# Kernel tuning notes

Measured on AMD Instinct MI355X. Metric: run time of the kernel, lower is better.

Reference implementation:

```python
import jax, jax.numpy as jnp
import numpy as np

C_IN = 256
C_RED = max(4, C_IN // 4)  # 64


def setup_inputs() -> dict:
    key = jax.random.key(0)
    k1, k2, k3, k4, k5 = jax.random.split(key, 5)
    B, C, H, W = 4, C_IN, 64, 64
    x = jax.random.normal(k1, (B, C, H, W), dtype=jnp.float32)
    # 1x1 convs (no bias) are just channel matmuls: weight shape (out_ch, in_ch)
    s_in = 1.0 / np.sqrt(C)
    s_red = 1.0 / np.sqrt(C_RED)
    Wq = jax.random.normal(k2, (C_RED, C), dtype=jnp.float32) * s_in
    Wk = jax.random.normal(k3, (C_RED, C), dtype=jnp.float32) * s_in
    Wv = jax.random.normal(k4, (C_RED, C), dtype=jnp.float32) * s_in
    Wp = jax.random.normal(k5, (C, C_RED), dtype=jnp.float32) * s_red
    return {"x": x, "Wq": Wq, "Wk": Wk, "Wv": Wv, "Wp": Wp}


def reference(x, Wq, Wk, Wv, Wp):
    B, C, H, W = x.shape
    N = H * W
    xf = x.reshape(B, C, N)                       # (B, C, N)
    q = jnp.einsum('rc,bcn->bnr', Wq, xf)         # (B, N, c_red)
    k = jnp.einsum('rc,bcn->brn', Wk, xf)         # (B, c_red, N)
    v = jnp.einsum('rc,bcn->bnr', Wv, xf)         # (B, N, c_red)
    scale = 1.0 / jnp.sqrt(jnp.float32(k.shape[1]))
    attn = jnp.einsum('bnr,brm->bnm', q, k) * scale   # (B, N, N)
    attn = jax.nn.softmax(attn, axis=-1)
    out = jnp.einsum('bnm,bmr->brn', attn, v)     # (B, c_red, N)
    out = jnp.einsum('cr,brn->bcn', Wp, out)      # (B, C, N)
    return out.reshape(B, C, H, W) + x
```

## Files before the change

### kernel.cpp

```cpp
#include <hip/hip_runtime.h>
#include <hip/hip_bf16.h>

#define CIN 256
#define CRED 64
#define NB 4
#define NN 4096

typedef float v4f __attribute__((ext_vector_type(4)));
typedef short v8s __attribute__((ext_vector_type(8)));
typedef unsigned short u16;
typedef u16 u16x4 __attribute__((ext_vector_type(4)));
typedef u16 u16x8 __attribute__((ext_vector_type(8)));
typedef unsigned int u32;

#define LOG2E 1.4426950408889634f

__device__ __forceinline__ u16 f2bf(float f) {
    union { float f; u32 u; } v; v.f = f;
    u32 r = (v.u + 0x7FFFu + ((v.u >> 16) & 1u)) >> 16;
    return (u16)r;
}
__device__ __forceinline__ float bf2f(u16 s) {
    union { u32 u; float f; } v; v.u = ((u32)s) << 16;
    return v.f;
}
__device__ __forceinline__ u32 pkbf(float a, float b) {
    float2 f; f.x = a; f.y = b;
    __hip_bfloat162 h = __float22bfloat162_rn(f);
    union { __hip_bfloat162 h; u32 u; } c; c.h = h;
    return c.u;
}
__device__ __forceinline__ v4f mfma16(v8s a, v8s b, v4f c) {
    return __builtin_amdgcn_mfma_f32_16x16x32_bf16(a, b, c, 0, 0, 0);
}
__device__ __forceinline__ float fexp2(float x) {
#if __has_builtin(__builtin_amdgcn_exp2f)
    return __builtin_amdgcn_exp2f(x);
#else
    return exp2f(x);
#endif
}

__global__ __launch_bounds__(256) void k_wconv(const float* __restrict__ Wq,
                                               const float* __restrict__ Wk,
                                               const float* __restrict__ Wv,
                                               const float* __restrict__ Wp,
                                               u16* __restrict__ Wb,
                                               u16* __restrict__ WpB) {
    int t = threadIdx.x;
    if (blockIdx.x < 48) {
        int idx = (blockIdx.x * 256 + t) * 4;
        int row = idx >> 8;
        int mat = row >> 6, r = row & 63, col = idx & 255;
        const float* src = (mat == 0) ? Wq : (mat == 1) ? Wk : Wv;
        float4 v = *(const float4*)&src[r * 256 + col];
        float s = (mat == 0) ? (0.125f * LOG2E) : 1.0f;
        u16x4 o;
        o[0] = f2bf(v.x * s); o[1] = f2bf(v.y * s);
        o[2] = f2bf(v.z * s); o[3] = f2bf(v.w * s);
        *(u16x4*)&Wb[idx] = o;
    } else {
        int idx = ((blockIdx.x - 48) * 256 + t) * 4;
        float4 v = *(const float4*)&Wp[idx];
        u16x4 o;
        o[0] = f2bf(v.x); o[1] = f2bf(v.y);
        o[2] = f2bf(v.z); o[3] = f2bf(v.w);
        *(u16x4*)&WpB[idx] = o;
    }
}

__global__ __launch_bounds__(256) void k_qkvm(const float* __restrict__ x,
                                              const u16* __restrict__ Wb,
                                              u16* __restrict__ Q, u16* __restrict__ K,
                                              u16* __restrict__ V) {
    int t = threadIdx.x;
    int wv = t >> 6, lane = t & 63, c15 = lane & 15, quad = lane >> 4;
    int n0g = blockIdx.x * 32;
    int b = n0g >> 12, nb = n0g & 4095;
    const float* xb = x + ((size_t)b << 20);

    v8s Af[2][8];
#pragma unroll
    for (int nt = 0; nt < 2; ++nt) {
        const float* px = xb + nb + nt * 16 + c15 + (size_t)quad * 8 * 4096;
#pragma unroll
        for (int kc = 0; kc < 8; ++kc) {
            float f[8];
#pragma unroll
            for (int j = 0; j < 8; ++j)
                f[j] = px[((size_t)kc * 32 + j) * 4096];
            union { v8s s; u32 w[4]; } pk;
            pk.w[0] = pkbf(f[0], f[1]); pk.w[1] = pkbf(f[2], f[3]);
            pk.w[2] = pkbf(f[4], f[5]); pk.w[3] = pkbf(f[6], f[7]);
            Af[nt][kc] = pk.s;
        }
    }

#pragma unroll
    for (int rti = 0; rti < 3; ++rti) {
        int rt = wv * 3 + rti;
        const u16* wrow = Wb + (size_t)(rt * 16 + c15) * 256 + quad * 8;
        v8s Bf[8];
#pragma unroll
        for (int kc = 0; kc < 8; ++kc) Bf[kc] = *(const v8s*)&wrow[kc * 32];
#pragma unroll
        for (int nt = 0; nt < 2; ++nt) {
            v4f acc = {0.f, 0.f, 0.f, 0.f};
#pragma unroll
            for (int kc = 0; kc < 8; ++kc)
                acc = mfma16(Af[nt][kc], Bf[kc], acc);
            if (rt < 8) {
                u16* base = (rt < 4) ? Q : K;
                u16* dst = base + ((size_t)b << 18)
                         + (size_t)(nb + nt * 16 + quad * 4) * 64
                         + (rt & 3) * 16 + c15;
#pragma unroll
                for (int g = 0; g < 4; ++g) dst[g * 64] = f2bf(acc[g]);
            } else {
                int hi2 = ((nb + nt * 16) >> 4) & 3;
                size_t base = ((size_t)b * 64 + (rt - 8) * 16 + c15) * 4096
                            + (size_t)((nb + nt * 16) & ~63) + hi2;
#pragma unroll
                for (int g = 0; g < 4; ++g)
                    V[base + (quad * 4 + g) * 4] = f2bf(acc[g]);
            }
        }
    }
}

__global__ __launch_bounds__(256, 4) void k_flash(const u16* __restrict__ Q,
                                                  const u16* __restrict__ K,
                                                  const u16* __restrict__ V,
                                                  u16* __restrict__ OP,
                                                  float* __restrict__ Lb,
                                                  int sh) {
    __shared__ u16 Kl[64][72];
    __shared__ u16 Vl[64][72];
    __shared__ u16 Pl[4][32][72];
    int t = threadIdx.x;
    int p = blockIdx.x & ((1u << sh) - 1);
    int tile = blockIdx.x >> sh;
    int b = tile >> 5;
    int n0 = (tile & 31) * 128;
    int wv = t >> 6;
    int lane = t & 63;
    int c15 = lane & 15;
    int quad = lane >> 4;
    int nw = n0 + wv * 32;
    const u16* Qb = Q + (size_t)b * NN * 64;
    const u16* Kb = K + (size_t)b * NN * 64;
    const u16* Vb = V + (size_t)b * 64 * NN;

    v8s Qa[2][2];
#pragma unroll
    for (int rg = 0; rg < 2; ++rg)
#pragma unroll
        for (int c2 = 0; c2 < 2; ++c2)
            Qa[rg][c2] = *(const v8s*)&Qb[(size_t)(nw + rg * 16 + c15) * 64 + c2 * 32 + quad * 8];

    v4f O[2][4];
    float ls[2][4];
#pragma unroll
    for (int rg = 0; rg < 2; ++rg)
#pragma unroll
        for (int g = 0; g < 4; ++g) {
            ls[rg][g] = 0.f;
#pragma unroll
            for (int cg = 0; cg < 4; ++cg) O[rg][cg][g] = 0.f;
        }

    int mlen = NN >> sh;
    int m0 = p * mlen;
    int iters = mlen >> 6;
    int srow = t >> 3, scol = (t & 7) * 8;

    v8s kpre[2], vpre[2];
#pragma unroll
    for (int pass = 0; pass < 2; ++pass) {
        int rr = srow + pass * 32;
        kpre[pass] = *(const v8s*)&Kb[(size_t)(m0 + rr) * 64 + scol];
        vpre[pass] = *(const v8s*)&Vb[(size_t)rr * NN + m0 + scol];
    }

    for (int it = 0; it < iters; ++it) {
#pragma unroll
        for (int pass = 0; pass < 2; ++pass) {
            int rr = srow + pass * 32;
            *(v8s*)&Kl[rr][scol] = kpre[pass];
            *(v8s*)&Vl[rr][scol] = vpre[pass];
        }
        __syncthreads();

        if (it + 1 < iters) {
            int mt = m0 + (it + 1) * 64;
#pragma unroll
            for (int pass = 0; pass < 2; ++pass) {
                int rr = srow + pass * 32;
                kpre[pass] = *(const v8s*)&Kb[(size_t)(mt + rr) * 64 + scol];
                vpre[pass] = *(const v8s*)&Vb[(size_t)rr * NN + mt + scol];
            }
        }

        v4f S[2][4];
#pragma unroll
        for (int rg = 0; rg < 2; ++rg)
#pragma unroll
            for (int s = 0; s < 4; ++s)
#pragma unroll
                for (int g = 0; g < 4; ++g) S[rg][s][g] = 0.f;
#pragma unroll
        for (int s = 0; s < 4; ++s)
#pragma unroll
            for (int c2 = 0; c2 < 2; ++c2) {
                v8s kb = *(const v8s*)&Kl[s * 16 + c15][c2 * 32 + quad * 8];
                S[0][s] = mfma16(Qa[0][c2], kb, S[0][s]);
                S[1][s] = mfma16(Qa[1][c2], kb, S[1][s]);
            }

#pragma unroll
        for (int rg = 0; rg < 2; ++rg) {
            float E[4][4];
#pragma unroll
            for (int s = 0; s < 4; ++s)
#pragma unroll
                for (int g = 0; g < 4; ++g) {
                    float e = fexp2(S[rg][s][g]);
                    E[s][g] = e;
                    ls[rg][g] += e;
                }
#pragma unroll
            for (int g = 0; g < 4; ++g) {
                union { u16x4 v; u32 w[2]; } p2;
                p2.w[0] = pkbf(E[0][g], E[1][g]);
                p2.w[1] = pkbf(E[2][g], E[3][g]);
                *(u16x4*)&Pl[wv][rg * 16 + quad * 4 + g][c15 * 4] = p2.v;
            }
        }

        v8s Pa[2][2];
#pragma unroll
        for (int rg = 0; rg < 2; ++rg)
#pragma unroll
            for (int c2 = 0; c2 < 2; ++c2)
                Pa[rg][c2] = *(const v8s*)&Pl[wv][rg * 16 + c15][c2 * 32 + quad * 8];
#pragma unroll
        for (int cg = 0; cg < 4; ++cg)
#pragma unroll
            for (int c2 = 0; c2 < 2; ++c2) {
                v8s vb = *(const v8s*)&Vl[cg * 16 + c15][c2 * 32 + quad * 8];
                O[0][cg] = mfma16(Pa[0][c2], vb, O[0][cg]);
                O[1][cg] = mfma16(Pa[1][c2], vb, O[1][cg]);
            }
        __syncthreads();
    }

    u16* OPp = OP + (size_t)p * (NB * NN * 64) + (size_t)b * NN * 64;
#pragma unroll
    for (int rg = 0; rg < 2; ++rg)
#pragma unroll
        for (int cg = 0; cg < 4; ++cg)
#pragma unroll
            for (int g = 0; g < 4; ++g) {
                int n = nw + rg * 16 + quad * 4 + g;
                OPp[(size_t)n * 64 + cg * 16 + c15] = f2bf(O[rg][cg][g]);
            }
#pragma unroll
    for (int rg = 0; rg < 2; ++rg)
#pragma unroll
        for (int g = 0; g < 4; ++g) {
            float v = ls[rg][g];
#pragma unroll
            for (int off = 1; off <= 8; off <<= 1) v += __shfl_xor(v, off);
            ls[rg][g] = v;
        }
    if (c15 == 0) {
        float* Lp = Lb + (size_t)p * (NB * NN) + (size_t)b * NN;
#pragma unroll
        for (int rg = 0; rg < 2; ++rg)
#pragma unroll
            for (int g = 0; g < 4; ++g) {
                int n = nw + rg * 16 + quad * 4 + g;
                Lp[n] = ls[rg][g];
            }
    }
}

#define OMP 72
__global__ __launch_bounds__(256) void k_proj(const u16* __restrict__ OP,
                                              const float* __restrict__ Lb,
                                              const u16* __restrict__ WpB,
                                              const float* __restrict__ x,
                                              float* __restrict__ out,
                                              int nsp) {
    __shared__ u16 Om[16 * OMP];
    int t = threadIdx.x;
    int b = blockIdx.x >> 8;
    int n0 = (blockIdx.x & 255) * 16;

    {
        int n_l = t >> 4, r0 = (t & 15) * 4;
        size_t nidx = (size_t)b * NN + n0 + n_l;
        float o[4] = {0.f, 0.f, 0.f, 0.f};
        float l = 0.f;
        for (int p = 0; p < nsp; ++p) {
            u16x4 u = *(const u16x4*)&OP[((size_t)p * (NB * NN) + nidx) * 64 + r0];
#pragma unroll
            for (int j = 0; j < 4; ++j) o[j] += bf2f(u[j]);
            l += Lb[(size_t)p * (NB * NN) + nidx];
        }
        float inv = 1.0f / l;
        union { u16x4 v; u32 w[2]; } p2;
        p2.w[0] = pkbf(o[0] * inv, o[1] * inv);
        p2.w[1] = pkbf(o[2] * inv, o[3] * inv);
        *(u16x4*)&Om[n_l * OMP + r0] = p2.v;
    }
    __syncthreads();

    int lane = t & 63, wvv = t >> 6, c15 = lane & 15, quad = lane >> 4;
    v8s B0 = *(const v8s*)&Om[c15 * OMP + quad * 8];
    v8s B1 = *(const v8s*)&Om[c15 * OMP + 32 + quad * 8];
#pragma unroll
    for (int ct0 = 0; ct0 < 4; ++ct0) {
        int ct = wvv * 4 + ct0;
        const u16* wrow = WpB + (size_t)(ct * 16 + c15) * 64 + quad * 8;
        v8s A0 = *(const v8s*)&wrow[0];
        v8s A1 = *(const v8s*)&wrow[32];
        v4f acc = {0.f, 0.f, 0.f, 0.f};
        acc = mfma16(A0, B0, acc);
        acc = mfma16(A1, B1, acc);
        size_t base = ((size_t)(b * 256 + ct * 16 + quad * 4)) * 4096 + n0 + c15;
#pragma unroll
        for (int g = 0; g < 4; ++g)
            out[base + (size_t)g * 4096] = acc[g] + x[base + (size_t)g * 4096];
    }
}

extern "C" void kernel_launch(void* const* d_in, const int* in_sizes, int n_in,
                              void* d_out, int out_size, void* d_ws, size_t ws_size,
                              hipStream_t stream) {
    const float* x  = (const float*)d_in[0];
    const float* Wq = (const float*)d_in[1];
    const float* Wk = (const float*)d_in[2];
    const float* Wv = (const float*)d_in[3];
    const float* Wp = (const float*)d_in[4];
    float* out = (float*)d_out;
    char* ws = (char*)d_ws;

    int nsp = (ws_size >= (size_t)24 * 1024 * 1024) ? 8 : 4;
    int sh = (nsp == 8) ? 3 : 2;

    u16* Wb  = (u16*)(ws);
    u16* WpB = (u16*)(ws + 131072);
    u16* Q   = (u16*)(ws + 262144);
    u16* K   = (u16*)(ws + 262144 + 2097152);
    u16* V   = (u16*)(ws + 262144 + 2 * 2097152);
    u16* OP  = (u16*)(ws + 262144 + 3 * 2097152);
    float* Lbuf = (float*)(ws + 262144 + (size_t)(3 + nsp) * 2097152);

    k_wconv<<<64, 256, 0, stream>>>(Wq, Wk, Wv, Wp, Wb, WpB);
    k_qkvm<<<512, 256, 0, stream>>>(x, Wb, Q, K, V);
    k_flash<<<NB * 32 * nsp, 256, 0, stream>>>(Q, K, V, OP, Lbuf, sh);
    k_proj<<<NB * 256, 256, 0, stream>>>(OP, Lbuf, WpB, x, out, nsp);
}
```

Baseline: 124.5 us.

## Double-buffer K/V via direct global-to-LDS loads and widen projection tiles

The flash kernel now stages K and V tiles straight into a double-buffered, XOR-swizzled LDS buffer with global_load_lds, in place of register prefetch followed by LDS stores. It also raises wave priority around the MFMA blocks and relaxes the occupancy hint to 3. The projection kernel handles 32 columns per block with a compile-time split count and converts Wp to bf16 on the fly, which removes that part of the weight-conversion kernel. The goal is to hide K/V load latency and cut LDS bank conflicts and register traffic, at the cost of more LDS per block and possibly lower occupancy.

```diff
diff --git a/kernel.cpp b/kernel.cpp
--- a/kernel.cpp
+++ b/kernel.cpp
@@ -44,29 +44,18 @@
 __global__ __launch_bounds__(256) void k_wconv(const float* __restrict__ Wq,
                                                const float* __restrict__ Wk,
                                                const float* __restrict__ Wv,
-                                               const float* __restrict__ Wp,
-                                               u16* __restrict__ Wb,
-                                               u16* __restrict__ WpB) {
+                                               u16* __restrict__ Wb) {
     int t = threadIdx.x;
-    if (blockIdx.x < 48) {
-        int idx = (blockIdx.x * 256 + t) * 4;
-        int row = idx >> 8;
-        int mat = row >> 6, r = row & 63, col = idx & 255;
-        const float* src = (mat == 0) ? Wq : (mat == 1) ? Wk : Wv;
-        float4 v = *(const float4*)&src[r * 256 + col];
-        float s = (mat == 0) ? (0.125f * LOG2E) : 1.0f;
-        u16x4 o;
-        o[0] = f2bf(v.x * s); o[1] = f2bf(v.y * s);
-        o[2] = f2bf(v.z * s); o[3] = f2bf(v.w * s);
-        *(u16x4*)&Wb[idx] = o;
-    } else {
-        int idx = ((blockIdx.x - 48) * 256 + t) * 4;
-        float4 v = *(const float4*)&Wp[idx];
-        u16x4 o;
-        o[0] = f2bf(v.x); o[1] = f2bf(v.y);
-        o[2] = f2bf(v.z); o[3] = f2bf(v.w);
-        *(u16x4*)&WpB[idx] = o;
-    }
+    int idx = (blockIdx.x * 256 + t) * 4;
+    int row = idx >> 8;
+    int mat = row >> 6, r = row & 63, col = idx & 255;
+    const float* src = (mat == 0) ? Wq : (mat == 1) ? Wk : Wv;
+    float4 v = *(const float4*)&src[r * 256 + col];
+    float s = (mat == 0) ? (0.125f * LOG2E) : 1.0f;
+    u16x4 o;
+    o[0] = f2bf(v.x * s); o[1] = f2bf(v.y * s);
+    o[2] = f2bf(v.z * s); o[3] = f2bf(v.w * s);
+    *(u16x4*)&Wb[idx] = o;
 }
 
 __global__ __launch_bounds__(256) void k_qkvm(const float* __restrict__ x,
@@ -128,15 +117,14 @@
     }
 }
 
-__global__ __launch_bounds__(256, 4) void k_flash(const u16* __restrict__ Q,
+__global__ __launch_bounds__(256, 3) void k_flash(const u16* __restrict__ Q,
                                                   const u16* __restrict__ K,
                                                   const u16* __restrict__ V,
                                                   u16* __restrict__ OP,
                                                   float* __restrict__ Lb,
                                                   int sh) {
-    __shared__ u16 Kl[64][72];
-    __shared__ u16 Vl[64][72];
-    __shared__ u16 Pl[4][32][72];
+    __shared__ __align__(16) u16 KV[2][2][4096];
+    __shared__ __align__(16) u16 Pl[4][32][72];
     int t = threadIdx.x;
     int p = blockIdx.x & ((1u << sh) - 1);
     int tile = blockIdx.x >> sh;
@@ -147,9 +135,9 @@
     int c15 = lane & 15;
     int quad = lane >> 4;
     int nw = n0 + wv * 32;
-    const u16* Qb = Q + (size_t)b * NN * 64;
-    const u16* Kb = K + (size_t)b * NN * 64;
-    const u16* Vb = V + (size_t)b * 64 * NN;
+    const u16* Qb = Q + ((size_t)b << 18);
+    const u16* Kb = K + ((size_t)b << 18);
+    const u16* Vb = V + ((size_t)b << 18);
 
     v8s Qa[2][2];
 #pragma unroll
@@ -172,34 +160,39 @@
     int mlen = NN >> sh;
     int m0 = p * mlen;
     int iters = mlen >> 6;
-    int srow = t >> 3, scol = (t & 7) * 8;
-
-    v8s kpre[2], vpre[2];
-#pragma unroll
-    for (int pass = 0; pass < 2; ++pass) {
-        int rr = srow + pass * 32;
-        kpre[pass] = *(const v8s*)&Kb[(size_t)(m0 + rr) * 64 + scol];
-        vpre[pass] = *(const v8s*)&Vb[(size_t)rr * NN + m0 + scol];
-    }
+
+    int lrow = lane >> 3;
+    int cs16 = (((lane & 7) ^ lrow) << 3);
+    const u16* gK = Kb + ((size_t)(wv * 16 + lrow) << 6) + cs16;
+    const u16* gV = Vb + ((size_t)(wv * 16 + lrow) << 12) + cs16;
+
+    auto stage = [&](int buf, int mt) {
+#pragma unroll
+        for (int i = 0; i < 2; ++i) {
+            __builtin_amdgcn_global_load_lds(
+                (const __attribute__((address_space(1))) void*)(gK + ((size_t)(mt + i * 8) << 6)),
+                (__attribute__((address_space(3))) void*)&KV[buf][0][(wv * 2 + i) << 9],
+                16, 0, 0);
+            __builtin_amdgcn_global_load_lds(
+                (const __attribute__((address_space(1))) void*)(gV + ((size_t)i << 15) + mt),
+                (__attribute__((address_space(3))) void*)&KV[buf][1][(wv * 2 + i) << 9],
+                16, 0, 0);
+        }
+    };
+
+    int swz = (c15 & 7) << 4;
+    int col0 = (quad << 4) ^ swz;
+    int col1 = col0 ^ 64;
+    int rbase = c15 << 7;
+
+    stage(0, m0);
+    __syncthreads();
 
     for (int it = 0; it < iters; ++it) {
-#pragma unroll
-        for (int pass = 0; pass < 2; ++pass) {
-            int rr = srow + pass * 32;
-            *(v8s*)&Kl[rr][scol] = kpre[pass];
-            *(v8s*)&Vl[rr][scol] = vpre[pass];
-        }
-        __syncthreads();
-
-        if (it + 1 < iters) {
-            int mt = m0 + (it + 1) * 64;
-#pragma unroll
-            for (int pass = 0; pass < 2; ++pass) {
-                int rr = srow + pass * 32;
-                kpre[pass] = *(const v8s*)&Kb[(size_t)(mt + rr) * 64 + scol];
-                vpre[pass] = *(const v8s*)&Vb[(size_t)rr * NN + mt + scol];
-            }
-        }
+        int cur = it & 1;
+        if (it + 1 < iters) stage(cur ^ 1, m0 + (it + 1) * 64);
+        const char* KB = (const char*)&KV[cur][0][0];
+        const char* VB = (const char*)&KV[cur][1][0];
 
         v4f S[2][4];
 #pragma unroll
@@ -208,14 +201,18 @@
             for (int s = 0; s < 4; ++s)
 #pragma unroll
                 for (int g = 0; g < 4; ++g) S[rg][s][g] = 0.f;
-#pragma unroll
-        for (int s = 0; s < 4; ++s)
-#pragma unroll
-            for (int c2 = 0; c2 < 2; ++c2) {
-                v8s kb = *(const v8s*)&Kl[s * 16 + c15][c2 * 32 + quad * 8];
-                S[0][s] = mfma16(Qa[0][c2], kb, S[0][s]);
-                S[1][s] = mfma16(Qa[1][c2], kb, S[1][s]);
-            }
+
+        __builtin_amdgcn_s_setprio(1);
+#pragma unroll
+        for (int s = 0; s < 4; ++s) {
+            v8s kb0 = *(const v8s*)(KB + rbase + s * 2048 + col0);
+            v8s kb1 = *(const v8s*)(KB + rbase + s * 2048 + col1);
+            S[0][s] = mfma16(Qa[0][0], kb0, S[0][s]);
+            S[1][s] = mfma16(Qa[1][0], kb0, S[1][s]);
+            S[0][s] = mfma16(Qa[0][1], kb1, S[0][s]);
+            S[1][s] = mfma16(Qa[1][1], kb1, S[1][s]);
+        }
+        __builtin_amdgcn_s_setprio(0);
 
 #pragma unroll
         for (int rg = 0; rg < 2; ++rg) {
@@ -243,14 +240,18 @@
 #pragma unroll
             for (int c2 = 0; c2 < 2; ++c2)
                 Pa[rg][c2] = *(const v8s*)&Pl[wv][rg * 16 + c15][c2 * 32 + quad * 8];
-#pragma unroll
-        for (int cg = 0; cg < 4; ++cg)
-#pragma unroll
-            for (int c2 = 0; c2 < 2; ++c2) {
-                v8s vb = *(const v8s*)&Vl[cg * 16 + c15][c2 * 32 + quad * 8];
-                O[0][cg] = mfma16(Pa[0][c2], vb, O[0][cg]);
-                O[1][cg] = mfma16(Pa[1][c2], vb, O[1][cg]);
-            }
+
+        __builtin_amdgcn_s_setprio(1);
+#pragma unroll
+        for (int cg = 0; cg < 4; ++cg) {
+            v8s vb0 = *(const v8s*)(VB + (cg << 11) + rbase + col0);
+            v8s vb1 = *(const v8s*)(VB + (cg << 11) + rbase + col1);
+            O[0][cg] = mfma16(Pa[0][0], vb0, O[0][cg]);
+            O[1][cg] = mfma16(Pa[1][0], vb0, O[1][cg]);
+            O[0][cg] = mfma16(Pa[0][1], vb1, O[0][cg]);
+            O[1][cg] = mfma16(Pa[1][1], vb1, O[1][cg]);
+        }
+        __builtin_amdgcn_s_setprio(0);
         __syncthreads();
     }
 
@@ -286,52 +287,69 @@
 }
 
 #define OMP 72
+template <int NSP>
 __global__ __launch_bounds__(256) void k_proj(const u16* __restrict__ OP,
                                               const float* __restrict__ Lb,
-                                              const u16* __restrict__ WpB,
+                                              const float* __restrict__ Wp,
                                               const float* __restrict__ x,
-                                              float* __restrict__ out,
-                                              int nsp) {
-    __shared__ u16 Om[16 * OMP];
+                                              float* __restrict__ out) {
+    __shared__ __align__(16) u16 Om[32 * OMP];
     int t = threadIdx.x;
-    int b = blockIdx.x >> 8;
-    int n0 = (blockIdx.x & 255) * 16;
+    int b = blockIdx.x >> 7;
+    int n0 = (blockIdx.x & 127) * 32;
 
     {
-        int n_l = t >> 4, r0 = (t & 15) * 4;
+        int n_l = t >> 3, r0 = (t & 7) * 8;
         size_t nidx = (size_t)b * NN + n0 + n_l;
-        float o[4] = {0.f, 0.f, 0.f, 0.f};
+        float o[8] = {0.f, 0.f, 0.f, 0.f, 0.f, 0.f, 0.f, 0.f};
         float l = 0.f;
-        for (int p = 0; p < nsp; ++p) {
-            u16x4 u = *(const u16x4*)&OP[((size_t)p * (NB * NN) + nidx) * 64 + r0];
-#pragma unroll
-            for (int j = 0; j < 4; ++j) o[j] += bf2f(u[j]);
+#pragma unroll
+        for (int p = 0; p < NSP; ++p) {
+            u16x8 u = *(const u16x8*)&OP[((size_t)p * (NB * NN) + nidx) * 64 + r0];
+#pragma unroll
+            for (int j = 0; j < 8; ++j) o[j] += bf2f(u[j]);
             l += Lb[(size_t)p * (NB * NN) + nidx];
         }
         float inv = 1.0f / l;
-        union { u16x4 v; u32 w[2]; } p2;
+        union { u16x8 v; u32 w[4]; } p2;
         p2.w[0] = pkbf(o[0] * inv, o[1] * inv);
         p2.w[1] = pkbf(o[2] * inv, o[3] * inv);
-        *(u16x4*)&Om[n_l * OMP + r0] = p2.v;
+        p2.w[2] = pkbf(o[4] * inv, o[5] * inv);
+        p2.w[3] = pkbf(o[6] * inv, o[7] * inv);
+        *(u16x8*)&Om[n_l * OMP + r0] = p2.v;
     }
     __syncthreads();
 
     int lane = t & 63, wvv = t >> 6, c15 = lane & 15, quad = lane >> 4;
-    v8s B0 = *(const v8s*)&Om[c15 * OMP + quad * 8];
-    v8s B1 = *(const v8s*)&Om[c15 * OMP + 32 + quad * 8];
+    v8s Bf[2][2];
+#pragma unroll
+    for (int nt = 0; nt < 2; ++nt) {
+        Bf[nt][0] = *(const v8s*)&Om[(nt * 16 + c15) * OMP + quad * 8];
+        Bf[nt][1] = *(const v8s*)&Om[(nt * 16 + c15) * OMP + 32 + quad * 8];
+    }
 #pragma unroll
     for (int ct0 = 0; ct0 < 4; ++ct0) {
         int ct = wvv * 4 + ct0;
-        const u16* wrow = WpB + (size_t)(ct * 16 + c15) * 64 + quad * 8;
-        v8s A0 = *(const v8s*)&wrow[0];
-        v8s A1 = *(const v8s*)&wrow[32];
-        v4f acc = {0.f, 0.f, 0.f, 0.f};
-        acc = mfma16(A0, B0, acc);
-        acc = mfma16(A1, B1, acc);
-        size_t base = ((size_t)(b * 256 + ct * 16 + quad * 4)) * 4096 + n0 + c15;
-#pragma unroll
-        for (int g = 0; g < 4; ++g)
-            out[base + (size_t)g * 4096] = acc[g] + x[base + (size_t)g * 4096];
+        const float* wrow = Wp + (size_t)(ct * 16 + c15) * 64 + quad * 8;
+        float4 wa = *(const float4*)&wrow[0];
+        float4 wb = *(const float4*)&wrow[4];
+        float4 wc = *(const float4*)&wrow[32];
+        float4 wd = *(const float4*)&wrow[36];
+        union { v8s s; u32 w[4]; } A0, A1;
+        A0.w[0] = pkbf(wa.x, wa.y); A0.w[1] = pkbf(wa.z, wa.w);
+        A0.w[2] = pkbf(wb.x, wb.y); A0.w[3] = pkbf(wb.z, wb.w);
+        A1.w[0] = pkbf(wc.x, wc.y); A1.w[1] = pkbf(wc.z, wc.w);
+        A1.w[2] = pkbf(wd.x, wd.y); A1.w[3] = pkbf(wd.z, wd.w);
+#pragma unroll
+        for (int nt = 0; nt < 2; ++nt) {
+            v4f acc = {0.f, 0.f, 0.f, 0.f};
+            acc = mfma16(A0.s, Bf[nt][0], acc);
+            acc = mfma16(A1.s, Bf[nt][1], acc);
+            size_t base = ((size_t)(b * 256 + ct * 16 + quad * 4)) * 4096 + n0 + nt * 16 + c15;
+#pragma unroll
+            for (int g = 0; g < 4; ++g)
+                out[base + (size_t)g * 4096] = acc[g] + x[base + (size_t)g * 4096];
+        }
     }
 }
 
@@ -350,15 +368,17 @@
     int sh = (nsp == 8) ? 3 : 2;
 
     u16* Wb  = (u16*)(ws);
-    u16* WpB = (u16*)(ws + 131072);
     u16* Q   = (u16*)(ws + 262144);
     u16* K   = (u16*)(ws + 262144 + 2097152);
     u16* V   = (u16*)(ws + 262144 + 2 * 2097152);
     u16* OP  = (u16*)(ws + 262144 + 3 * 2097152);
     float* Lbuf = (float*)(ws + 262144 + (size_t)(3 + nsp) * 2097152);
 
-    k_wconv<<<64, 256, 0, stream>>>(Wq, Wk, Wv, Wp, Wb, WpB);
+    k_wconv<<<48, 256, 0, stream>>>(Wq, Wk, Wv, Wb);
     k_qkvm<<<512, 256, 0, stream>>>(x, Wb, Q, K, V);
     k_flash<<<NB * 32 * nsp, 256, 0, stream>>>(Q, K, V, OP, Lbuf, sh);
-    k_proj<<<NB * 256, 256, 0, stream>>>(OP, Lbuf, WpB, x, out, nsp);
-}
+    if (nsp == 8)
+        k_proj<8><<<NB * 128, 256, 0, stream>>>(OP, Lbuf, Wp, x, out);
+    else
+        k_proj<4><<<NB * 128, 256, 0, stream>>>(OP, Lbuf, Wp, x, out);
+}
```

Result: no change. 122.7 us (-1.4%).
